# Kernel optimization log

Hardware: AMD Instinct MI355X
Metric: run time of the kernel (lower is better)

Reference implementation:

```python
import jax, jax.numpy as jnp
import numpy as np

D_MODEL = 1024
H = 16
D_HEAD = D_MODEL // H  # 64
RANK = 32
ALPHA = 1.0


def _lora_linear(x, W, b, dW, dB):
    # merged weight: W + alpha * (dB @ dW), then x @ W_merged.T + b
    Wm = W + ALPHA * (dB @ dW)
    return x @ Wm.T + b


def setup_inputs() -> dict:
    key = jax.random.key(0)
    ks = jax.random.split(key, 20)
    inp = {"x": jax.random.normal(ks[0], (2, 2048, D_MODEL), dtype=jnp.float32)}
    i = 1
    for name in ("q", "k", "v", "o"):
        inp[f"{name}_W"] = jax.random.normal(ks[i], (D_MODEL, D_MODEL), dtype=jnp.float32) * 0.02; i += 1
        inp[f"{name}_b"] = jnp.zeros((D_MODEL,), dtype=jnp.float32)
        inp[f"{name}_dW"] = jax.random.normal(ks[i], (RANK, D_MODEL), dtype=jnp.float32) * 0.01; i += 1
        inp[f"{name}_dB"] = jax.random.normal(ks[i], (D_MODEL, RANK), dtype=jnp.float32) * 0.01; i += 1
    return inp


def reference(x, q_W, q_b, q_dW, q_dB, k_W, k_b, k_dW, k_dB,
              v_W, v_b, v_dW, v_dB, o_W, o_b, o_dW, o_dB):
    b_s, n, _ = x.shape
    # LoRA-merged QKV projections
    q = _lora_linear(x, q_W, q_b, q_dW, q_dB).reshape(b_s, n, H, D_HEAD)
    k = _lora_linear(x, k_W, k_b, k_dW, k_dB).reshape(b_s, n, H, D_HEAD)
    v = _lora_linear(x, v_W, v_b, v_dW, v_dB).reshape(b_s, n, H, D_HEAD)
    scale = 1.0 / np.sqrt(D_HEAD).astype(np.float32)
    # att: [b, h, nq, nk]
    att = jnp.einsum('bqhd,bkhd->bhqk', q, k) * scale
    att = jax.nn.softmax(att, axis=-1)  # dropout = identity (eval mode)
    out = jnp.einsum('bhqk,bkhd->bqhd', att, v).reshape(b_s, n, H * D_HEAD)
    return _lora_linear(out, o_W, o_b, o_dW, o_dB)
```

## Files before the change

### kernel.cpp

```cpp
#include <hip/hip_runtime.h>

typedef unsigned short ushort_t;
typedef unsigned int u32;
typedef __attribute__((ext_vector_type(8))) short short8;
typedef __attribute__((ext_vector_type(4))) float floatx4;

typedef const __attribute__((address_space(1))) u32* gptr_t;
typedef __attribute__((address_space(3))) u32* lptr_t;

__device__ __forceinline__ void async_copy16(void* lds, const void* g) {
  __builtin_amdgcn_global_load_lds((gptr_t)g, (lptr_t)lds, 16, 0, 0);
}

__device__ __forceinline__ ushort_t f2bf(float f) {
  u32 u = __float_as_uint(f);
  u += 0x7fffu + ((u >> 16) & 1u);
  return (ushort_t)(u >> 16);
}

__device__ __forceinline__ floatx4 mfma16(short8 a, short8 b, floatx4 c) {
  return __builtin_amdgcn_mfma_f32_16x16x32_bf16(a, b, c, 0, 0, 0);
}

struct alignas(16) F4 { float a, b, c, d; };
struct alignas(8) U4 { ushort_t a, b, c, d; };

#define QSCALE 0.18033688011112043f

__global__ __launch_bounds__(256) void prep_kernel(
    const float* __restrict__ x, ushort_t* __restrict__ xs,
    const float* __restrict__ W0, const float* __restrict__ dW0, const float* __restrict__ dB0,
    const float* __restrict__ W1, const float* __restrict__ dW1, const float* __restrict__ dB1,
    const float* __restrict__ W2, const float* __restrict__ dW2, const float* __restrict__ dB2,
    const float* __restrict__ W3, const float* __restrict__ dW3, const float* __restrict__ dB3,
    ushort_t* __restrict__ Wm) {
  const int bid = blockIdx.x;
  if (bid < 4096) {
    int i = bid * 256 + threadIdx.x;
    F4 v = ((const F4*)x)[i];
    U4 hh = {f2bf(v.a), f2bf(v.b), f2bf(v.c), f2bf(v.d)};
    ((U4*)xs)[i] = hh;
    return;
  }
  const int t = bid - 4096;
  const int layer = t >> 7, sub = t & 127;
  const float* W = (layer == 0) ? W0 : (layer == 1) ? W1 : (layer == 2) ? W2 : W3;
  const float* dW = (layer == 0) ? dW0 : (layer == 1) ? dW1 : (layer == 2) ? dW2 : dW3;
  const float* dB = (layer == 0) ? dB0 : (layer == 1) ? dB1 : (layer == 2) ? dB2 : dB3;
  ushort_t* Wh = Wm + (size_t)layer * 1024 * 1024;
  const int ot = sub * 8;
  const int d0 = threadIdx.x * 4;
  float acc[8][4] = {};
  for (int r = 0; r < 32; ++r) {
    F4 w = *(const F4*)&dW[r * 1024 + d0];
    float wv[4] = {w.a, w.b, w.c, w.d};
#pragma unroll
    for (int o = 0; o < 8; ++o) {
      float s = dB[(ot + o) * 32 + r];
#pragma unroll
      for (int j = 0; j < 4; ++j) acc[o][j] += s * wv[j];
    }
  }
#pragma unroll
  for (int o = 0; o < 8; ++o) {
    F4 w = *(const F4*)&W[(ot + o) * 1024 + d0];
    U4 hh = {f2bf(w.a + acc[o][0]), f2bf(w.b + acc[o][1]),
             f2bf(w.c + acc[o][2]), f2bf(w.d + acc[o][3])};
    *(U4*)&Wh[(ot + o) * 1024 + d0] = hh;
  }
}

template <int MODE, int TN>
__global__ __launch_bounds__(256) void gemm_bt(
    const ushort_t* __restrict__ A, const ushort_t* __restrict__ B,
    const float* __restrict__ b0, const float* __restrict__ b1,
    const float* __restrict__ b2,
    ushort_t* __restrict__ C, ushort_t* __restrict__ vth,
    float* __restrict__ Cf, const int M, const int N, const int K) {
  constexpr int NT2 = TN / 32;
  __shared__ __align__(16) ushort_t lA[2][128 * 32], lB[2][TN * 32];
  const int tid = threadIdx.x;
  const int wave = tid >> 6, lane = tid & 63;
  const int lo4 = lane & 15, quad = lane >> 4;
  const int n0 = blockIdx.x * TN, m0 = blockIdx.y * 128;
  const int wm = (wave >> 1) * 64, wn = (wave & 1) * (TN / 2);

  floatx4 acc[4][NT2];
  const floatx4 zero4 = {0.f, 0.f, 0.f, 0.f};
#pragma unroll
  for (int mt = 0; mt < 4; ++mt)
#pragma unroll
    for (int nt = 0; nt < NT2; ++nt) acc[mt][nt] = zero4;

  const int strow = lane >> 2;
  const int stcol = (lane & 3) * 8;

  const int NTILES = K >> 5;
  {
#pragma unroll
    for (int i = 0; i < 2; ++i) {
      const int g = wave * 2 + i;
      async_copy16(&lA[0][g * 512], A + (size_t)(m0 + g * 16 + strow) * K + stcol);
    }
#pragma unroll
    for (int i = 0; i < TN / 64; ++i) {
      const int g = wave * (TN / 64) + i;
      async_copy16(&lB[0][g * 512], B + (size_t)(n0 + g * 16 + strow) * K + stcol);
    }
  }
  __syncthreads();

  for (int t = 0; t < NTILES; ++t) {
    const int cur = t & 1;
    if (t + 1 < NTILES) {
      const int kk = (t + 1) << 5;
#pragma unroll
      for (int i = 0; i < 2; ++i) {
        const int g = wave * 2 + i;
        async_copy16(&lA[cur ^ 1][g * 512], A + (size_t)(m0 + g * 16 + strow) * K + kk + stcol);
      }
#pragma unroll
      for (int i = 0; i < TN / 64; ++i) {
        const int g = wave * (TN / 64) + i;
        async_copy16(&lB[cur ^ 1][g * 512], B + (size_t)(n0 + g * 16 + strow) * K + kk + stcol);
      }
    }
    short8 a_[4], b_[NT2];
#pragma unroll
    for (int t2 = 0; t2 < 4; ++t2)
      a_[t2] = *(const short8*)&lA[cur][(wm + t2 * 16 + lo4) * 32 + quad * 8];
#pragma unroll
    for (int t2 = 0; t2 < NT2; ++t2)
      b_[t2] = *(const short8*)&lB[cur][(wn + t2 * 16 + lo4) * 32 + quad * 8];
#pragma unroll
    for (int mt = 0; mt < 4; ++mt)
#pragma unroll
      for (int nt = 0; nt < NT2; ++nt) acc[mt][nt] = mfma16(a_[mt], b_[nt], acc[mt][nt]);
    if (t + 1 < NTILES) __syncthreads();
  }

#pragma unroll
  for (int nt = 0; nt < NT2; ++nt) {
    const int col = n0 + wn + nt * 16 + lo4;
    float bias;
    if (MODE == 0)
      bias = (col < 1024) ? b0[col] : (col < 2048) ? b1[col - 1024] : b2[col - 2048];
    else
      bias = b0[col];
#pragma unroll
    for (int mt = 0; mt < 4; ++mt)
#pragma unroll
      for (int r = 0; r < 4; ++r) {
        const int row = m0 + wm + mt * 16 + quad * 4 + r;
        float c = acc[mt][nt][r] + bias;
        if (MODE == 0) {
          if (col < 1024) c *= QSCALE;
          ushort_t hv = f2bf(c);
          if (col < 2048) {
            C[(size_t)row * 2048 + col] = hv;
          } else {
            const int d = col - 2048;
            const size_t vrow = (size_t)(((row >> 11) * 16 + (d >> 6)) * 64 + (d & 63));
            vth[vrow * 2048 + (row & 2047)] = hv;
          }
        } else {
          Cf[(size_t)row * N + col] = c;
        }
      }
  }
}

__global__ __launch_bounds__(512) void attn_kernel(
    const ushort_t* __restrict__ qk, const ushort_t* __restrict__ vt,
    ushort_t* __restrict__ at) {
  __shared__ __align__(16) ushort_t Kh[2][64 * 64], Vh[2][64 * 64];
  __shared__ __align__(16) ushort_t P[8][16][72];
  const int qt = blockIdx.x, bh = blockIdx.y;
  const int b = bh >> 4, h = bh & 15;
  const int tid = threadIdx.x;
  const int wave = tid >> 6, lane = tid & 63;
  const int lo4 = lane & 15, quad = lane >> 4;

  short8 qh[2];
  {
    const size_t g = (size_t)(b * 2048 + qt * 128 + wave * 16 + lo4) * 2048 + h * 64 + quad * 8;
    qh[0] = *(const short8*)(qk + g);
    qh[1] = *(const short8*)(qk + g + 32);
  }
  float l_acc[4] = {0.f, 0.f, 0.f, 0.f};
  const floatx4 zero4 = {0.f, 0.f, 0.f, 0.f};
  floatx4 O[4];
#pragma unroll
  for (int nt = 0; nt < 4; ++nt) O[nt] = zero4;

  const int strow = lane >> 3;
  const int stcol = ((lane & 7) ^ strow) * 8;
  const int srow = wave * 8 + strow;
  const int uoff = wave * 8 * 64;

  async_copy16(&Kh[0][uoff], qk + (size_t)(b * 2048 + srow) * 2048 + 1024 + h * 64 + stcol);
  async_copy16(&Vh[0][uoff], vt + (size_t)(bh * 64 + srow) * 2048 + stcol);
  __syncthreads();

  for (int kt = 0; kt < 32; ++kt) {
    const int cur = kt & 1;
    if (kt + 1 < 32) {
      const int kn = (kt + 1) * 64;
      async_copy16(&Kh[cur ^ 1][uoff],
                   qk + (size_t)(b * 2048 + kn + srow) * 2048 + 1024 + h * 64 + stcol);
      async_copy16(&Vh[cur ^ 1][uoff], vt + (size_t)(bh * 64 + srow) * 2048 + kn + stcol);
    }

    floatx4 s[4];
#pragma unroll
    for (int nt = 0; nt < 4; ++nt) s[nt] = zero4;
#pragma unroll
    for (int nt = 0; nt < 4; ++nt)
#pragma unroll
      for (int ks = 0; ks < 2; ++ks) {
        const int off = (nt * 16 + lo4) * 64 + (((ks * 4 + quad) ^ (lo4 & 7)) * 8);
        s[nt] = mfma16(qh[ks], *(const short8*)&Kh[cur][off], s[nt]);
      }

#pragma unroll
    for (int nt = 0; nt < 4; ++nt)
#pragma unroll
      for (int r = 0; r < 4; ++r) {
        float pv = __builtin_amdgcn_exp2f(s[nt][r]);
        s[nt][r] = pv;
        P[wave][quad * 4 + r][nt * 16 + lo4] = (ushort_t)(__float_as_uint(pv) >> 16);
      }
#pragma unroll
    for (int r = 0; r < 4; ++r)
      l_acc[r] += (s[0][r] + s[1][r]) + (s[2][r] + s[3][r]);

#pragma unroll
    for (int ks = 0; ks < 2; ++ks) {
      short8 pf = *(const short8*)&P[wave][lo4][ks * 32 + quad * 8];
#pragma unroll
      for (int nt = 0; nt < 4; ++nt) {
        const int off = (nt * 16 + lo4) * 64 + (((ks * 4 + quad) ^ (lo4 & 7)) * 8);
        O[nt] = mfma16(pf, *(const short8*)&Vh[cur][off], O[nt]);
      }
    }
    if (kt + 1 < 32) __syncthreads();
  }

  float linv[4];
#pragma unroll
  for (int r = 0; r < 4; ++r) {
    float s = l_acc[r];
    s += __shfl_xor(s, 1);
    s += __shfl_xor(s, 2);
    s += __shfl_xor(s, 4);
    s += __shfl_xor(s, 8);
    linv[r] = 1.f / s;
  }
#pragma unroll
  for (int nt = 0; nt < 4; ++nt)
#pragma unroll
    for (int r = 0; r < 4; ++r) {
      float o = O[nt][r] * linv[r];
      const size_t row = (size_t)(b * 2048 + qt * 128 + wave * 16 + quad * 4 + r);
      at[row * 1024 + h * 64 + nt * 16 + lo4] = f2bf(o);
    }
}

extern "C" void kernel_launch(void* const* d_in, const int* in_sizes, int n_in,
                              void* d_out, int out_size, void* d_ws, size_t ws_size,
                              hipStream_t stream) {
  const float* x = (const float*)d_in[0];
  const float* qW = (const float*)d_in[1];
  const float* qb = (const float*)d_in[2];
  const float* qdW = (const float*)d_in[3];
  const float* qdB = (const float*)d_in[4];
  const float* kW = (const float*)d_in[5];
  const float* kb = (const float*)d_in[6];
  const float* kdW = (const float*)d_in[7];
  const float* kdB = (const float*)d_in[8];
  const float* vW = (const float*)d_in[9];
  const float* vb = (const float*)d_in[10];
  const float* vdW = (const float*)d_in[11];
  const float* vdB = (const float*)d_in[12];
  const float* oW = (const float*)d_in[13];
  const float* ob = (const float*)d_in[14];
  const float* odW = (const float*)d_in[15];
  const float* odB = (const float*)d_in[16];

  char* ws = (char*)d_ws;
  const size_t MB = 1024u * 1024u;
  const size_t WELEM = 1024u * 1024u;
  ushort_t* xs = (ushort_t*)(ws + 0 * MB);
  ushort_t* Wm = (ushort_t*)(ws + 8 * MB);
  ushort_t* qk = (ushort_t*)(ws + 16 * MB);
  ushort_t* vt = (ushort_t*)(ws + 32 * MB);
  ushort_t* at = xs;

  prep_kernel<<<4608, 256, 0, stream>>>(x, xs, qW, qdW, qdB, kW, kdW, kdB,
                                        vW, vdW, vdB, oW, odW, odB, Wm);
  gemm_bt<0, 128><<<dim3(24, 32), 256, 0, stream>>>(xs, Wm, qb, kb, vb,
                                                    qk, vt, nullptr, 4096, 3072, 1024);
  attn_kernel<<<dim3(16, 32), 512, 0, stream>>>(qk, vt, at);
  gemm_bt<1, 64><<<dim3(16, 32), 256, 0, stream>>>(at, Wm + 3 * WELEM, ob, nullptr,
                                                   nullptr, nullptr, nullptr,
                                                   (float*)d_out, 4096, 1024, 1024);
}
```

Before: 232.8 us.

## Compute V transposed via separate GEMM and double query rows per attention wave

The V projection is split out of the fused QKV GEMM into its own launch that computes V^T directly as W_v·x^T per batch. This replaces the scattered transposed 2-byte stores with row-contiguous stores. The attention kernel drops to 256 threads, with each wave handling 32 query rows instead of 16. Each K and V fragment read from LDS is then reused by two MFMAs, halving LDS traffic per MFMA. The cost is one extra kernel launch and more registers per wave in attention.

```diff
diff --git a/kernel.cpp b/kernel.cpp
--- a/kernel.cpp
+++ b/kernel.cpp
@@ -74,9 +74,8 @@
 __global__ __launch_bounds__(256) void gemm_bt(
     const ushort_t* __restrict__ A, const ushort_t* __restrict__ B,
     const float* __restrict__ b0, const float* __restrict__ b1,
-    const float* __restrict__ b2,
-    ushort_t* __restrict__ C, ushort_t* __restrict__ vth,
-    float* __restrict__ Cf, const int M, const int N, const int K) {
+    ushort_t* __restrict__ C, float* __restrict__ Cf,
+    const int M, const int N, const int K) {
   constexpr int NT2 = TN / 32;
   __shared__ __align__(16) ushort_t lA[2][128 * 32], lB[2][TN * 32];
   const int tid = threadIdx.x;
@@ -85,6 +84,11 @@
   const int n0 = blockIdx.x * TN, m0 = blockIdx.y * 128;
   const int wm = (wave >> 1) * 64, wn = (wave & 1) * (TN / 2);
 
+  if (MODE == 2) {
+    B += (size_t)blockIdx.z * 2048 * 1024;
+    C += (size_t)blockIdx.z * 1024 * 2048;
+  }
+
   floatx4 acc[4][NT2];
   const floatx4 zero4 = {0.f, 0.f, 0.f, 0.f};
 #pragma unroll
@@ -142,27 +146,20 @@
 #pragma unroll
   for (int nt = 0; nt < NT2; ++nt) {
     const int col = n0 + wn + nt * 16 + lo4;
-    float bias;
-    if (MODE == 0)
-      bias = (col < 1024) ? b0[col] : (col < 2048) ? b1[col - 1024] : b2[col - 2048];
-    else
-      bias = b0[col];
+    float cbias = 0.f;
+    if (MODE == 0) cbias = (col < 1024) ? b0[col] : b1[col - 1024];
+    if (MODE == 1) cbias = b0[col];
 #pragma unroll
     for (int mt = 0; mt < 4; ++mt)
 #pragma unroll
       for (int r = 0; r < 4; ++r) {
         const int row = m0 + wm + mt * 16 + quad * 4 + r;
-        float c = acc[mt][nt][r] + bias;
+        float c = acc[mt][nt][r] + (MODE == 2 ? b0[row] : cbias);
         if (MODE == 0) {
           if (col < 1024) c *= QSCALE;
-          ushort_t hv = f2bf(c);
-          if (col < 2048) {
-            C[(size_t)row * 2048 + col] = hv;
-          } else {
-            const int d = col - 2048;
-            const size_t vrow = (size_t)(((row >> 11) * 16 + (d >> 6)) * 64 + (d & 63));
-            vth[vrow * 2048 + (row & 2047)] = hv;
-          }
+          C[(size_t)row * 2048 + col] = f2bf(c);
+        } else if (MODE == 2) {
+          C[(size_t)row * 2048 + col] = f2bf(c);
         } else {
           Cf[(size_t)row * N + col] = c;
         }
@@ -170,100 +167,127 @@
   }
 }
 
-__global__ __launch_bounds__(512) void attn_kernel(
+__global__ __launch_bounds__(256) void attn_kernel(
     const ushort_t* __restrict__ qk, const ushort_t* __restrict__ vt,
     ushort_t* __restrict__ at) {
   __shared__ __align__(16) ushort_t Kh[2][64 * 64], Vh[2][64 * 64];
-  __shared__ __align__(16) ushort_t P[8][16][72];
+  __shared__ __align__(16) ushort_t P[4][32][68];
   const int qt = blockIdx.x, bh = blockIdx.y;
   const int b = bh >> 4, h = bh & 15;
   const int tid = threadIdx.x;
   const int wave = tid >> 6, lane = tid & 63;
   const int lo4 = lane & 15, quad = lane >> 4;
 
-  short8 qh[2];
-  {
-    const size_t g = (size_t)(b * 2048 + qt * 128 + wave * 16 + lo4) * 2048 + h * 64 + quad * 8;
-    qh[0] = *(const short8*)(qk + g);
-    qh[1] = *(const short8*)(qk + g + 32);
-  }
-  float l_acc[4] = {0.f, 0.f, 0.f, 0.f};
+  short8 qh[2][2];
+#pragma unroll
+  for (int mt = 0; mt < 2; ++mt) {
+    const size_t g =
+        (size_t)(b * 2048 + qt * 128 + wave * 32 + mt * 16 + lo4) * 2048 + h * 64 + quad * 8;
+    qh[mt][0] = *(const short8*)(qk + g);
+    qh[mt][1] = *(const short8*)(qk + g + 32);
+  }
+  float l_acc[2][4] = {};
   const floatx4 zero4 = {0.f, 0.f, 0.f, 0.f};
-  floatx4 O[4];
-#pragma unroll
-  for (int nt = 0; nt < 4; ++nt) O[nt] = zero4;
+  floatx4 O[2][4];
+#pragma unroll
+  for (int mt = 0; mt < 2; ++mt)
+#pragma unroll
+    for (int nt = 0; nt < 4; ++nt) O[mt][nt] = zero4;
 
   const int strow = lane >> 3;
   const int stcol = ((lane & 7) ^ strow) * 8;
-  const int srow = wave * 8 + strow;
-  const int uoff = wave * 8 * 64;
-
-  async_copy16(&Kh[0][uoff], qk + (size_t)(b * 2048 + srow) * 2048 + 1024 + h * 64 + stcol);
-  async_copy16(&Vh[0][uoff], vt + (size_t)(bh * 64 + srow) * 2048 + stcol);
+
+#pragma unroll
+  for (int i = 0; i < 2; ++i) {
+    const int row = wave * 16 + i * 8 + strow;
+    const int uoff = (wave * 16 + i * 8) * 64;
+    async_copy16(&Kh[0][uoff], qk + (size_t)(b * 2048 + row) * 2048 + 1024 + h * 64 + stcol);
+    async_copy16(&Vh[0][uoff], vt + (size_t)(bh * 64 + row) * 2048 + stcol);
+  }
   __syncthreads();
 
   for (int kt = 0; kt < 32; ++kt) {
     const int cur = kt & 1;
     if (kt + 1 < 32) {
       const int kn = (kt + 1) * 64;
-      async_copy16(&Kh[cur ^ 1][uoff],
-                   qk + (size_t)(b * 2048 + kn + srow) * 2048 + 1024 + h * 64 + stcol);
-      async_copy16(&Vh[cur ^ 1][uoff], vt + (size_t)(bh * 64 + srow) * 2048 + kn + stcol);
-    }
-
-    floatx4 s[4];
-#pragma unroll
-    for (int nt = 0; nt < 4; ++nt) s[nt] = zero4;
+#pragma unroll
+      for (int i = 0; i < 2; ++i) {
+        const int row = wave * 16 + i * 8 + strow;
+        const int uoff = (wave * 16 + i * 8) * 64;
+        async_copy16(&Kh[cur ^ 1][uoff],
+                     qk + (size_t)(b * 2048 + kn + row) * 2048 + 1024 + h * 64 + stcol);
+        async_copy16(&Vh[cur ^ 1][uoff], vt + (size_t)(bh * 64 + row) * 2048 + kn + stcol);
+      }
+    }
+
+    floatx4 s[2][4];
+#pragma unroll
+    for (int mt = 0; mt < 2; ++mt)
+#pragma unroll
+      for (int nt = 0; nt < 4; ++nt) s[mt][nt] = zero4;
 #pragma unroll
     for (int nt = 0; nt < 4; ++nt)
 #pragma unroll
       for (int ks = 0; ks < 2; ++ks) {
         const int off = (nt * 16 + lo4) * 64 + (((ks * 4 + quad) ^ (lo4 & 7)) * 8);
-        s[nt] = mfma16(qh[ks], *(const short8*)&Kh[cur][off], s[nt]);
-      }
-
-#pragma unroll
-    for (int nt = 0; nt < 4; ++nt)
-#pragma unroll
-      for (int r = 0; r < 4; ++r) {
-        float pv = __builtin_amdgcn_exp2f(s[nt][r]);
-        s[nt][r] = pv;
-        P[wave][quad * 4 + r][nt * 16 + lo4] = (ushort_t)(__float_as_uint(pv) >> 16);
-      }
-#pragma unroll
-    for (int r = 0; r < 4; ++r)
-      l_acc[r] += (s[0][r] + s[1][r]) + (s[2][r] + s[3][r]);
+        short8 kf = *(const short8*)&Kh[cur][off];
+        s[0][nt] = mfma16(qh[0][ks], kf, s[0][nt]);
+        s[1][nt] = mfma16(qh[1][ks], kf, s[1][nt]);
+      }
+
+#pragma unroll
+    for (int mt = 0; mt < 2; ++mt) {
+#pragma unroll
+      for (int nt = 0; nt < 4; ++nt)
+#pragma unroll
+        for (int r = 0; r < 4; ++r) {
+          float pv = __builtin_amdgcn_exp2f(s[mt][nt][r]);
+          s[mt][nt][r] = pv;
+          P[wave][mt * 16 + quad * 4 + r][nt * 16 + lo4] =
+              (ushort_t)(__float_as_uint(pv) >> 16);
+        }
+#pragma unroll
+      for (int r = 0; r < 4; ++r)
+        l_acc[mt][r] += (s[mt][0][r] + s[mt][1][r]) + (s[mt][2][r] + s[mt][3][r]);
+    }
 
 #pragma unroll
     for (int ks = 0; ks < 2; ++ks) {
-      short8 pf = *(const short8*)&P[wave][lo4][ks * 32 + quad * 8];
+      short8 pf0 = *(const short8*)&P[wave][lo4][ks * 32 + quad * 8];
+      short8 pf1 = *(const short8*)&P[wave][16 + lo4][ks * 32 + quad * 8];
 #pragma unroll
       for (int nt = 0; nt < 4; ++nt) {
         const int off = (nt * 16 + lo4) * 64 + (((ks * 4 + quad) ^ (lo4 & 7)) * 8);
-        O[nt] = mfma16(pf, *(const short8*)&Vh[cur][off], O[nt]);
+        short8 vf = *(const short8*)&Vh[cur][off];
+        O[0][nt] = mfma16(pf0, vf, O[0][nt]);
+        O[1][nt] = mfma16(pf1, vf, O[1][nt]);
       }
     }
     if (kt + 1 < 32) __syncthreads();
   }
 
-  float linv[4];
-#pragma unroll
-  for (int r = 0; r < 4; ++r) {
-    float s = l_acc[r];
-    s += __shfl_xor(s, 1);
-    s += __shfl_xor(s, 2);
-    s += __shfl_xor(s, 4);
-    s += __shfl_xor(s, 8);
-    linv[r] = 1.f / s;
-  }
-#pragma unroll
-  for (int nt = 0; nt < 4; ++nt)
+#pragma unroll
+  for (int mt = 0; mt < 2; ++mt) {
+    float linv[4];
 #pragma unroll
     for (int r = 0; r < 4; ++r) {
-      float o = O[nt][r] * linv[r];
-      const size_t row = (size_t)(b * 2048 + qt * 128 + wave * 16 + quad * 4 + r);
-      at[row * 1024 + h * 64 + nt * 16 + lo4] = f2bf(o);
-    }
+      float s = l_acc[mt][r];
+      s += __shfl_xor(s, 1);
+      s += __shfl_xor(s, 2);
+      s += __shfl_xor(s, 4);
+      s += __shfl_xor(s, 8);
+      linv[r] = 1.f / s;
+    }
+#pragma unroll
+    for (int nt = 0; nt < 4; ++nt)
+#pragma unroll
+      for (int r = 0; r < 4; ++r) {
+        float o = O[mt][nt][r] * linv[r];
+        const size_t row =
+            (size_t)(b * 2048 + qt * 128 + wave * 32 + mt * 16 + quad * 4 + r);
+        at[row * 1024 + h * 64 + nt * 16 + lo4] = f2bf(o);
+      }
+  }
 }
 
 extern "C" void kernel_launch(void* const* d_in, const int* in_sizes, int n_in,
@@ -298,10 +322,12 @@
 
   prep_kernel<<<4608, 256, 0, stream>>>(x, xs, qW, qdW, qdB, kW, kdW, kdB,
                                         vW, vdW, vdB, oW, odW, odB, Wm);
-  gemm_bt<0, 128><<<dim3(24, 32), 256, 0, stream>>>(xs, Wm, qb, kb, vb,
-                                                    qk, vt, nullptr, 4096, 3072, 1024);
-  attn_kernel<<<dim3(16, 32), 512, 0, stream>>>(qk, vt, at);
+  gemm_bt<0, 128><<<dim3(16, 32), 256, 0, stream>>>(xs, Wm, qb, kb, qk, nullptr,
+                                                    4096, 2048, 1024);
+  gemm_bt<2, 128><<<dim3(16, 8, 2), 256, 0, stream>>>(Wm + 2 * WELEM, xs, vb, nullptr,
+                                                      vt, nullptr, 1024, 2048, 1024);
+  attn_kernel<<<dim3(16, 32), 256, 0, stream>>>(qk, vt, at);
   gemm_bt<1, 64><<<dim3(16, 32), 256, 0, stream>>>(at, Wm + 3 * WELEM, ob, nullptr,
-                                                   nullptr, nullptr, nullptr,
-                                                   (float*)d_out, 4096, 1024, 1024);
-}
+                                                   nullptr, (float*)d_out,
+                                                   4096, 1024, 1024);
+}
```

Measured after the change: 250.4 us. 1.08x slower.

## Split QKV GEMM, compute V transposed via swapped operands, tile K/V contiguously per head

Applied to the files above, without the earlier changes.

The fused QKV GEMM is split so Q and K come from x·Wᵀ while V is computed as Wv·xᵀ, which writes V already transposed without the scattered column stores. K and V are stored per head in contiguous 64x64 tiles, so the attention kernel's async loads read contiguous 8KB chunks instead of strided rows. The attention grid is reordered with heads on x, so blocks sharing a head's K/V run close together. The GEMMs are specialised with fixed dimensions, and the V blocks' output tiles are now strided to match the new layout.

```diff
diff --git a/kernel.cpp b/kernel.cpp
--- a/kernel.cpp
+++ b/kernel.cpp
@@ -70,112 +70,182 @@
   }
 }
 
-template <int MODE, int TN>
-__global__ __launch_bounds__(256) void gemm_bt(
-    const ushort_t* __restrict__ A, const ushort_t* __restrict__ B,
-    const float* __restrict__ b0, const float* __restrict__ b1,
-    const float* __restrict__ b2,
-    ushort_t* __restrict__ C, ushort_t* __restrict__ vth,
-    float* __restrict__ Cf, const int M, const int N, const int K) {
-  constexpr int NT2 = TN / 32;
-  __shared__ __align__(16) ushort_t lA[2][128 * 32], lB[2][TN * 32];
+__global__ __launch_bounds__(256) void gemm_qkvt(
+    const ushort_t* __restrict__ xs, const ushort_t* __restrict__ Wm,
+    const float* __restrict__ qb, const float* __restrict__ kb,
+    const float* __restrict__ vb,
+    ushort_t* __restrict__ qx, ushort_t* __restrict__ kx,
+    ushort_t* __restrict__ vt) {
+  __shared__ __align__(16) ushort_t lA[2][128 * 32], lB[2][128 * 32];
   const int tid = threadIdx.x;
   const int wave = tid >> 6, lane = tid & 63;
   const int lo4 = lane & 15, quad = lane >> 4;
-  const int n0 = blockIdx.x * TN, m0 = blockIdx.y * 128;
-  const int wm = (wave >> 1) * 64, wn = (wave & 1) * (TN / 2);
-
-  floatx4 acc[4][NT2];
+  const int n0 = blockIdx.x * 128;
+  const int wm = (wave >> 1) * 64, wn = (wave & 1) * 64;
+
+  const bool isVT = blockIdx.y >= 32;
+  const ushort_t* A;
+  const ushort_t* B;
+  int m0, z = 0;
+  if (!isVT) {
+    A = xs;
+    B = Wm;
+    m0 = blockIdx.y * 128;
+  } else {
+    const int t = blockIdx.y - 32;
+    z = t >> 3;
+    A = Wm + 2u * 1024 * 1024;
+    B = xs + (size_t)z * 2048 * 1024;
+    m0 = (t & 7) * 128;
+  }
+
+  floatx4 acc[4][4];
   const floatx4 zero4 = {0.f, 0.f, 0.f, 0.f};
 #pragma unroll
   for (int mt = 0; mt < 4; ++mt)
 #pragma unroll
-    for (int nt = 0; nt < NT2; ++nt) acc[mt][nt] = zero4;
+    for (int nt = 0; nt < 4; ++nt) acc[mt][nt] = zero4;
 
   const int strow = lane >> 2;
   const int stcol = (lane & 3) * 8;
 
-  const int NTILES = K >> 5;
   {
 #pragma unroll
     for (int i = 0; i < 2; ++i) {
       const int g = wave * 2 + i;
-      async_copy16(&lA[0][g * 512], A + (size_t)(m0 + g * 16 + strow) * K + stcol);
-    }
-#pragma unroll
-    for (int i = 0; i < TN / 64; ++i) {
-      const int g = wave * (TN / 64) + i;
-      async_copy16(&lB[0][g * 512], B + (size_t)(n0 + g * 16 + strow) * K + stcol);
+      async_copy16(&lA[0][g * 512], A + (size_t)(m0 + g * 16 + strow) * 1024 + stcol);
+      async_copy16(&lB[0][g * 512], B + (size_t)(n0 + g * 16 + strow) * 1024 + stcol);
     }
   }
   __syncthreads();
 
-  for (int t = 0; t < NTILES; ++t) {
+  for (int t = 0; t < 32; ++t) {
     const int cur = t & 1;
-    if (t + 1 < NTILES) {
+    if (t + 1 < 32) {
       const int kk = (t + 1) << 5;
 #pragma unroll
       for (int i = 0; i < 2; ++i) {
         const int g = wave * 2 + i;
-        async_copy16(&lA[cur ^ 1][g * 512], A + (size_t)(m0 + g * 16 + strow) * K + kk + stcol);
-      }
-#pragma unroll
-      for (int i = 0; i < TN / 64; ++i) {
-        const int g = wave * (TN / 64) + i;
-        async_copy16(&lB[cur ^ 1][g * 512], B + (size_t)(n0 + g * 16 + strow) * K + kk + stcol);
-      }
-    }
-    short8 a_[4], b_[NT2];
+        async_copy16(&lA[cur ^ 1][g * 512], A + (size_t)(m0 + g * 16 + strow) * 1024 + kk + stcol);
+        async_copy16(&lB[cur ^ 1][g * 512], B + (size_t)(n0 + g * 16 + strow) * 1024 + kk + stcol);
+      }
+    }
+    short8 a_[4], b_[4];
+#pragma unroll
+    for (int t2 = 0; t2 < 4; ++t2) {
+      a_[t2] = *(const short8*)&lA[cur][(wm + t2 * 16 + lo4) * 32 + quad * 8];
+      b_[t2] = *(const short8*)&lB[cur][(wn + t2 * 16 + lo4) * 32 + quad * 8];
+    }
+#pragma unroll
+    for (int mt = 0; mt < 4; ++mt)
+#pragma unroll
+      for (int nt = 0; nt < 4; ++nt) acc[mt][nt] = mfma16(a_[mt], b_[nt], acc[mt][nt]);
+    if (t + 1 < 32) __syncthreads();
+  }
+
+#pragma unroll
+  for (int nt = 0; nt < 4; ++nt) {
+    const int col = n0 + wn + nt * 16 + lo4;
+#pragma unroll
+    for (int mt = 0; mt < 4; ++mt)
+#pragma unroll
+      for (int r = 0; r < 4; ++r) {
+        const int row = m0 + wm + mt * 16 + quad * 4 + r;
+        if (!isVT) {
+          float c = acc[mt][nt][r] + ((col < 1024) ? qb[col] : kb[col - 1024]);
+          if (col < 1024) {
+            c *= QSCALE;
+            qx[(size_t)row * 1024 + col] = f2bf(c);
+          } else {
+            const int d = col - 1024;
+            kx[(size_t)((row >> 11) * 16 + (d >> 6)) * 131072 + (size_t)(row & 2047) * 64 +
+               (d & 63)] = f2bf(c);
+          }
+        } else {
+          float c = acc[mt][nt][r] + vb[row];
+          vt[(size_t)(((z * 16 + (row >> 6)) * 32 + (col >> 6)) * 4096) +
+             (size_t)(row & 63) * 64 + (col & 63)] = f2bf(c);
+        }
+      }
+  }
+}
+
+__global__ __launch_bounds__(256) void gemm_out(
+    const ushort_t* __restrict__ A, const ushort_t* __restrict__ B,
+    const float* __restrict__ bias, float* __restrict__ Cf) {
+  __shared__ __align__(16) ushort_t lA[2][128 * 32], lB[2][64 * 32];
+  const int tid = threadIdx.x;
+  const int wave = tid >> 6, lane = tid & 63;
+  const int lo4 = lane & 15, quad = lane >> 4;
+  const int n0 = blockIdx.x * 64, m0 = blockIdx.y * 128;
+  const int wm = (wave >> 1) * 64, wn = (wave & 1) * 32;
+
+  floatx4 acc[4][2];
+  const floatx4 zero4 = {0.f, 0.f, 0.f, 0.f};
+#pragma unroll
+  for (int mt = 0; mt < 4; ++mt)
+#pragma unroll
+    for (int nt = 0; nt < 2; ++nt) acc[mt][nt] = zero4;
+
+  const int strow = lane >> 2;
+  const int stcol = (lane & 3) * 8;
+
+  {
+#pragma unroll
+    for (int i = 0; i < 2; ++i) {
+      const int g = wave * 2 + i;
+      async_copy16(&lA[0][g * 512], A + (size_t)(m0 + g * 16 + strow) * 1024 + stcol);
+    }
+    async_copy16(&lB[0][wave * 512], B + (size_t)(n0 + wave * 16 + strow) * 1024 + stcol);
+  }
+  __syncthreads();
+
+  for (int t = 0; t < 32; ++t) {
+    const int cur = t & 1;
+    if (t + 1 < 32) {
+      const int kk = (t + 1) << 5;
+#pragma unroll
+      for (int i = 0; i < 2; ++i) {
+        const int g = wave * 2 + i;
+        async_copy16(&lA[cur ^ 1][g * 512], A + (size_t)(m0 + g * 16 + strow) * 1024 + kk + stcol);
+      }
+      async_copy16(&lB[cur ^ 1][wave * 512],
+                   B + (size_t)(n0 + wave * 16 + strow) * 1024 + kk + stcol);
+    }
+    short8 a_[4], b_[2];
 #pragma unroll
     for (int t2 = 0; t2 < 4; ++t2)
       a_[t2] = *(const short8*)&lA[cur][(wm + t2 * 16 + lo4) * 32 + quad * 8];
 #pragma unroll
-    for (int t2 = 0; t2 < NT2; ++t2)
+    for (int t2 = 0; t2 < 2; ++t2)
       b_[t2] = *(const short8*)&lB[cur][(wn + t2 * 16 + lo4) * 32 + quad * 8];
 #pragma unroll
     for (int mt = 0; mt < 4; ++mt)
 #pragma unroll
-      for (int nt = 0; nt < NT2; ++nt) acc[mt][nt] = mfma16(a_[mt], b_[nt], acc[mt][nt]);
-    if (t + 1 < NTILES) __syncthreads();
-  }
-
-#pragma unroll
-  for (int nt = 0; nt < NT2; ++nt) {
+      for (int nt = 0; nt < 2; ++nt) acc[mt][nt] = mfma16(a_[mt], b_[nt], acc[mt][nt]);
+    if (t + 1 < 32) __syncthreads();
+  }
+
+#pragma unroll
+  for (int nt = 0; nt < 2; ++nt) {
     const int col = n0 + wn + nt * 16 + lo4;
-    float bias;
-    if (MODE == 0)
-      bias = (col < 1024) ? b0[col] : (col < 2048) ? b1[col - 1024] : b2[col - 2048];
-    else
-      bias = b0[col];
+    const float cb = bias[col];
 #pragma unroll
     for (int mt = 0; mt < 4; ++mt)
 #pragma unroll
       for (int r = 0; r < 4; ++r) {
         const int row = m0 + wm + mt * 16 + quad * 4 + r;
-        float c = acc[mt][nt][r] + bias;
-        if (MODE == 0) {
-          if (col < 1024) c *= QSCALE;
-          ushort_t hv = f2bf(c);
-          if (col < 2048) {
-            C[(size_t)row * 2048 + col] = hv;
-          } else {
-            const int d = col - 2048;
-            const size_t vrow = (size_t)(((row >> 11) * 16 + (d >> 6)) * 64 + (d & 63));
-            vth[vrow * 2048 + (row & 2047)] = hv;
-          }
-        } else {
-          Cf[(size_t)row * N + col] = c;
-        }
+        Cf[(size_t)row * 1024 + col] = acc[mt][nt][r] + cb;
       }
   }
 }
 
 __global__ __launch_bounds__(512) void attn_kernel(
-    const ushort_t* __restrict__ qk, const ushort_t* __restrict__ vt,
-    ushort_t* __restrict__ at) {
+    const ushort_t* __restrict__ qx, const ushort_t* __restrict__ kx,
+    const ushort_t* __restrict__ vt, ushort_t* __restrict__ at) {
   __shared__ __align__(16) ushort_t Kh[2][64 * 64], Vh[2][64 * 64];
   __shared__ __align__(16) ushort_t P[8][16][72];
-  const int qt = blockIdx.x, bh = blockIdx.y;
+  const int bh = blockIdx.x, qt = blockIdx.y;
   const int b = bh >> 4, h = bh & 15;
   const int tid = threadIdx.x;
   const int wave = tid >> 6, lane = tid & 63;
@@ -183,9 +253,9 @@
 
   short8 qh[2];
   {
-    const size_t g = (size_t)(b * 2048 + qt * 128 + wave * 16 + lo4) * 2048 + h * 64 + quad * 8;
-    qh[0] = *(const short8*)(qk + g);
-    qh[1] = *(const short8*)(qk + g + 32);
+    const size_t g = (size_t)(b * 2048 + qt * 128 + wave * 16 + lo4) * 1024 + h * 64 + quad * 8;
+    qh[0] = *(const short8*)(qx + g);
+    qh[1] = *(const short8*)(qx + g + 32);
   }
   float l_acc[4] = {0.f, 0.f, 0.f, 0.f};
   const floatx4 zero4 = {0.f, 0.f, 0.f, 0.f};
@@ -194,21 +264,23 @@
   for (int nt = 0; nt < 4; ++nt) O[nt] = zero4;
 
   const int strow = lane >> 3;
-  const int stcol = ((lane & 7) ^ strow) * 8;
+  const int csw = ((lane & 7) ^ strow) * 8;
+  const size_t kbase = (size_t)bh * 131072;
+  const size_t vbase = (size_t)bh * 32 * 4096;
   const int srow = wave * 8 + strow;
-  const int uoff = wave * 8 * 64;
-
-  async_copy16(&Kh[0][uoff], qk + (size_t)(b * 2048 + srow) * 2048 + 1024 + h * 64 + stcol);
-  async_copy16(&Vh[0][uoff], vt + (size_t)(bh * 64 + srow) * 2048 + stcol);
+  const int uoff = wave * 512;
+
+  async_copy16(&Kh[0][uoff], kx + kbase + (size_t)srow * 64 + csw);
+  async_copy16(&Vh[0][uoff], vt + vbase + (size_t)srow * 64 + csw);
   __syncthreads();
 
   for (int kt = 0; kt < 32; ++kt) {
     const int cur = kt & 1;
     if (kt + 1 < 32) {
-      const int kn = (kt + 1) * 64;
       async_copy16(&Kh[cur ^ 1][uoff],
-                   qk + (size_t)(b * 2048 + kn + srow) * 2048 + 1024 + h * 64 + stcol);
-      async_copy16(&Vh[cur ^ 1][uoff], vt + (size_t)(bh * 64 + srow) * 2048 + kn + stcol);
+                   kx + kbase + (size_t)((kt + 1) * 64 + srow) * 64 + csw);
+      async_copy16(&Vh[cur ^ 1][uoff],
+                   vt + vbase + (size_t)(kt + 1) * 4096 + (size_t)srow * 64 + csw);
     }
 
     floatx4 s[4];
@@ -292,16 +364,14 @@
   const size_t WELEM = 1024u * 1024u;
   ushort_t* xs = (ushort_t*)(ws + 0 * MB);
   ushort_t* Wm = (ushort_t*)(ws + 8 * MB);
-  ushort_t* qk = (ushort_t*)(ws + 16 * MB);
+  ushort_t* qx = (ushort_t*)(ws + 16 * MB);
+  ushort_t* kx = (ushort_t*)(ws + 24 * MB);
   ushort_t* vt = (ushort_t*)(ws + 32 * MB);
   ushort_t* at = xs;
 
   prep_kernel<<<4608, 256, 0, stream>>>(x, xs, qW, qdW, qdB, kW, kdW, kdB,
                                         vW, vdW, vdB, oW, odW, odB, Wm);
-  gemm_bt<0, 128><<<dim3(24, 32), 256, 0, stream>>>(xs, Wm, qb, kb, vb,
-                                                    qk, vt, nullptr, 4096, 3072, 1024);
-  attn_kernel<<<dim3(16, 32), 512, 0, stream>>>(qk, vt, at);
-  gemm_bt<1, 64><<<dim3(16, 32), 256, 0, stream>>>(at, Wm + 3 * WELEM, ob, nullptr,
-                                                   nullptr, nullptr, nullptr,
-                                                   (float*)d_out, 4096, 1024, 1024);
-}
+  gemm_qkvt<<<dim3(16, 48), 256, 0, stream>>>(xs, Wm, qb, kb, vb, qx, kx, vt);
+  attn_kernel<<<dim3(32, 16), 512, 0, stream>>>(qx, kx, vt, at);
+  gemm_out<<<dim3(16, 32), 256, 0, stream>>>(at, Wm + 3 * WELEM, ob, (float*)d_out);
+}
```

Result: no change. 236.1 us (+1.4%).
